# Kernel tuning notes

Hardware: AMD Instinct MI355X
Metric: run time of the kernel (lower is better)

Reference implementation:

```python
import jax, jax.numpy as jnp
import numpy as np

N_NODES = 100000
N_EDGES = 1600000
IN_DIM = 128
HID = 128
N_CLS = 10
N_GRAPHS = 128


def setup_inputs() -> dict:
    key = jax.random.key(0)
    ks = jax.random.split(key, 8)
    x = jax.random.normal(ks[0], (N_NODES, IN_DIM), dtype=jnp.float32)
    edge_index = jax.random.randint(ks[1], (2, N_EDGES), 0, N_NODES, dtype=jnp.int64)
    batch = jnp.sort(jax.random.randint(ks[2], (N_NODES,), 0, N_GRAPHS, dtype=jnp.int64))
    # GCNConv weights (PyG uses glorot; scale approximated) and biases
    W1 = jax.random.normal(ks[3], (IN_DIM, HID), dtype=jnp.float32) * (1.0 / np.sqrt(IN_DIM))
    b1 = jnp.zeros((HID,), dtype=jnp.float32)
    W2 = jax.random.normal(ks[4], (HID, HID), dtype=jnp.float32) * (1.0 / np.sqrt(HID))
    b2 = jnp.zeros((HID,), dtype=jnp.float32)
    Wlin = jax.random.normal(ks[5], (HID, N_CLS), dtype=jnp.float32) * (1.0 / np.sqrt(HID))
    blin = jnp.zeros((N_CLS,), dtype=jnp.float32)
    return {"x": x, "edge_index": edge_index, "batch": batch,
            "W1": W1, "b1": b1, "W2": W2, "b2": b2, "Wlin": Wlin, "blin": blin}


def _gcn_norm(edge_index, n_nodes):
    # PyG GCNConv default: add self-loops, symmetric D^-1/2 A D^-1/2 normalization
    loop = jnp.arange(n_nodes, dtype=edge_index.dtype)
    row = jnp.concatenate([edge_index[0], loop])  # source nodes
    col = jnp.concatenate([edge_index[1], loop])  # destination nodes
    ones = jnp.ones(col.shape[0], dtype=jnp.float32)
    deg = jax.ops.segment_sum(ones, col, num_segments=n_nodes)
    dinv = jnp.where(deg > 0, jax.lax.rsqrt(deg), 0.0)
    norm = dinv[row] * dinv[col]  # per-edge normalization coefficient
    return row, col, norm


def _gcn_conv(x, W, b, row, col, norm, n_nodes):
    h = x @ W                                   # [N, hid] dense transform first (small hid)
    msg = h[row] * norm[:, None]                # gather + scale over edges
    out = jax.ops.segment_sum(msg, col, num_segments=n_nodes)  # scatter-add aggregation
    return out + b


def reference(x, edge_index, batch, W1, b1, W2, b2, Wlin, blin):
    n = x.shape[0]
    row, col, norm = _gcn_norm(edge_index, n)
    h = jax.nn.relu(_gcn_conv(x, W1, b1, row, col, norm, n))
    h = jax.nn.relu(_gcn_conv(h, W2, b2, row, col, norm, n))
    # global_mean_pool over batch ids
    sums = jax.ops.segment_sum(h, batch, num_segments=N_GRAPHS)
    cnts = jax.ops.segment_sum(jnp.ones((n,), dtype=h.dtype), batch, num_segments=N_GRAPHS)
    pooled = sums / jnp.maximum(cnts, 1.0)[:, None]
    return pooled @ Wlin + blin  # [N_GRAPHS, n_cls]
```

## Files before the change

### kernel.cpp

```cpp
#include <hip/hip_runtime.h>

#define NN 100000
#define NE 1600000
#define DD 128
#define NG 128
#define NC 10
#define POOL_WAVES 2048

#define B1SH 8
#define NB1 ((NN + 255) / 256)
#define EPB 8192
#define NWG1 ((NE + EPB - 1) / EPB)

typedef __attribute__((ext_vector_type(8))) short short8v;
typedef __attribute__((ext_vector_type(4))) float f32x4;

__device__ __forceinline__ unsigned short f2bf(float f) {
    unsigned int u = __float_as_uint(f);
    u = (u + 0x7fffu + ((u >> 16) & 1u)) >> 16;
    return (unsigned short)u;
}

__global__ __launch_bounds__(256) void hist_k(const int* __restrict__ col, int* __restrict__ hist) {
    __shared__ int lh[NB1];
    int t = threadIdx.x, w = blockIdx.x;
    for (int i = t; i < NB1; i += 256) lh[i] = 0;
    __syncthreads();
    int base = w * EPB;
    int lim = min(base + EPB, NE);
#pragma unroll 4
    for (int e = base + t; e < lim; e += 256) atomicAdd(&lh[col[e] >> B1SH], 1);
    __syncthreads();
    for (int i = t; i < NB1; i += 256) hist[i * NWG1 + w] = lh[i];
}

__global__ __launch_bounds__(512) void btot_k(const int* __restrict__ hist, int* __restrict__ bbase) {
    __shared__ int tmp[512];
    int t = threadIdx.x;
    int s = 0;
    if (t < NB1) {
        const int* hp = hist + t * NWG1;
        for (int w = 0; w < NWG1; ++w) s += hp[w];
    }
    tmp[t] = s;
    __syncthreads();
    for (int o = 1; o < 512; o <<= 1) {
        int v = (t >= o) ? tmp[t - o] : 0;
        __syncthreads();
        tmp[t] += v;
        __syncthreads();
    }
    if (t < NB1) bbase[t] = tmp[t] - s;
    if (t == 511) bbase[NB1] = tmp[511];
}

__global__ __launch_bounds__(256) void histscan_k(const int* __restrict__ bbase, int* __restrict__ hist) {
    __shared__ int tmp[256];
    int b = blockIdx.x, t = threadIdx.x;
    int v = (t < NWG1) ? hist[b * NWG1 + t] : 0;
    tmp[t] = v;
    __syncthreads();
    for (int o = 1; o < 256; o <<= 1) {
        int u = (t >= o) ? tmp[t - o] : 0;
        __syncthreads();
        tmp[t] += u;
        __syncthreads();
    }
    int excl = tmp[t] - v;
    if (t < NWG1) hist[b * NWG1 + t] = bbase[b] + excl;
}

__global__ __launch_bounds__(256) void part1_k(const int* __restrict__ row, const int* __restrict__ col,
                                               const int* __restrict__ hist, int* __restrict__ tmpe) {
    __shared__ int lcur[NB1];
    int t = threadIdx.x, w = blockIdx.x;
    for (int i = t; i < NB1; i += 256) lcur[i] = hist[i * NWG1 + w];
    __syncthreads();
    int base = w * EPB;
    int lim = min(base + EPB, NE);
#pragma unroll 4
    for (int e = base + t; e < lim; e += 256) {
        int c = col[e];
        int pos = atomicAdd(&lcur[c >> B1SH], 1);
        tmpe[pos] = (row[e] << B1SH) | (c & 255);
    }
}

__global__ __launch_bounds__(512) void part2b_k(const int* __restrict__ bbase, const int* __restrict__ tmpe,
                                                unsigned int* __restrict__ csr_src, int* __restrict__ offs,
                                                float* __restrict__ dinv) {
    __shared__ int lcnt[256];
    __shared__ int lsc[256];
    int b = blockIdx.x, t = threadIdx.x;
    if (t < 256) lcnt[t] = 0;
    __syncthreads();
    int ebeg = bbase[b], eend = bbase[b + 1];
    for (int e = ebeg + t; e < eend; e += 512) atomicAdd(&lcnt[tmpe[e] & 255], 1);
    __syncthreads();
    if (t < 256) lsc[t] = lcnt[t];
    __syncthreads();
    for (int o = 1; o < 256; o <<= 1) {
        int v = (t < 256 && t >= o) ? lsc[t - o] : 0;
        __syncthreads();
        if (t < 256) lsc[t] += v;
        __syncthreads();
    }
    int n0 = b << B1SH;
    if (t < 256) {
        int node = n0 + t;
        if (node < NN) {
            int excl = lsc[t] - lcnt[t];
            offs[node] = ebeg + excl;
            dinv[node] = rsqrtf((float)lcnt[t] + 1.0f);
        }
    }
    if (b == NB1 - 1 && t == 0) offs[NN] = NE;
    __syncthreads();
    if (t < 256) lsc[t] = ebeg + (lsc[t] - lcnt[t]);
    __syncthreads();
    for (int e = ebeg + t; e < eend; e += 512) {
        int p = tmpe[e];
        int pos = atomicAdd(&lsc[p & 255], 1);
        csr_src[pos] = (unsigned int)(p >> B1SH) << 6;
    }
}

__global__ __launch_bounds__(256) void pack_w2_k(const float* __restrict__ W1, const float* __restrict__ W2,
                                                 unsigned short* __restrict__ Wpk1,
                                                 unsigned short* __restrict__ Wpk2) {
    const float* W = blockIdx.x ? W2 : W1;
    unsigned short* Wpk = blockIdx.x ? Wpk2 : Wpk1;
    int t = threadIdx.x;
    for (int f = t * 64; f < t * 64 + 64; ++f) {
        int j = f & 7, lane = (f >> 3) & 63, kk = (f >> 9) & 3, n = f >> 11;
        int k = kk * 32 + ((lane >> 4) << 3) + j;
        int c = n * 16 + (lane & 15);
        Wpk[f] = f2bf(W[k * DD + c]);
    }
}

template <int IN_BF16>
__global__ __launch_bounds__(256) void gemm_mfma_k(const void* __restrict__ Xv,
                                                   const unsigned short* __restrict__ Wpk,
                                                   const float* __restrict__ dinv,
                                                   unsigned short* __restrict__ outb) {
    __shared__ unsigned short wlds[16384];
    int tid = threadIdx.x;
    const uint4* wg = (const uint4*)Wpk;
    uint4* wl = (uint4*)wlds;
#pragma unroll
    for (int i = 0; i < 8; ++i) wl[tid + i * 256] = wg[tid + i * 256];
    __syncthreads();

    int w = tid >> 6, lane = tid & 63;
    int kg = lane >> 4;
    int rowbase = blockIdx.x * 64 + w * 16;
    int rl = min(rowbase + (lane & 15), NN - 1);

    short8v a[4];
    if (IN_BF16) {
        const unsigned short* xb = (const unsigned short*)Xv;
#pragma unroll
        for (int kk = 0; kk < 4; ++kk)
            a[kk] = *(const short8v*)(xb + (long)rl * DD + kk * 32 + kg * 8);
    } else {
        const float* xf = (const float*)Xv;
#pragma unroll
        for (int kk = 0; kk < 4; ++kk) {
            float4 f0 = *(const float4*)(xf + (long)rl * DD + kk * 32 + kg * 8);
            float4 f1 = *(const float4*)(xf + (long)rl * DD + kk * 32 + kg * 8 + 4);
            short8v t;
            t[0] = (short)f2bf(f0.x); t[1] = (short)f2bf(f0.y);
            t[2] = (short)f2bf(f0.z); t[3] = (short)f2bf(f0.w);
            t[4] = (short)f2bf(f1.x); t[5] = (short)f2bf(f1.y);
            t[6] = (short)f2bf(f1.z); t[7] = (short)f2bf(f1.w);
            a[kk] = t;
        }
    }

    f32x4 acc[8];
#pragma unroll
    for (int n = 0; n < 8; ++n) acc[n] = (f32x4){0.f, 0.f, 0.f, 0.f};
#pragma unroll
    for (int n = 0; n < 8; ++n) {
#pragma unroll
        for (int kk = 0; kk < 4; ++kk) {
            short8v b = *(const short8v*)(wlds + ((n * 4 + kk) * 64 + lane) * 8);
            acc[n] = __builtin_amdgcn_mfma_f32_16x16x32_bf16(a[kk], b, acc[n], 0, 0, 0);
        }
    }

    int c0 = lane & 15;
#pragma unroll
    for (int reg = 0; reg < 4; ++reg) {
        int row = rowbase + kg * 4 + reg;
        if (row < NN) {
            float dv = dinv[row];
            unsigned short* op = outb + (long)row * DD + c0;
#pragma unroll
            for (int n = 0; n < 8; ++n) op[n * 16] = f2bf(dv * acc[n][reg]);
        }
    }
}

__global__ __launch_bounds__(256) void agg_k(const unsigned int* __restrict__ hpb,
                                             const float* __restrict__ dinv,
                                             const int* __restrict__ offs,
                                             const unsigned int* __restrict__ csr,
                                             const float* __restrict__ bias,
                                             unsigned short* __restrict__ outb) {
    int node = (blockIdx.x << 2) + (threadIdx.x >> 6);
    if (node >= NN) return;
    unsigned int lane = threadIdx.x & 63;
    int s = offs[node];
    int e_end = offs[node + 1];
    unsigned int ps = hpb[(unsigned int)node * 64u + lane];
    float accx = __uint_as_float(ps << 16);
    float accy = __uint_as_float(ps & 0xffff0000u);
    int e = s;
    for (; e + 8 <= e_end; e += 8) {
        unsigned int i0 = csr[e] + lane;     unsigned int i1 = csr[e + 1] + lane;
        unsigned int i2 = csr[e + 2] + lane; unsigned int i3 = csr[e + 3] + lane;
        unsigned int i4 = csr[e + 4] + lane; unsigned int i5 = csr[e + 5] + lane;
        unsigned int i6 = csr[e + 6] + lane; unsigned int i7 = csr[e + 7] + lane;
        unsigned int p0 = hpb[i0];
        unsigned int p1 = hpb[i1];
        unsigned int p2 = hpb[i2];
        unsigned int p3 = hpb[i3];
        unsigned int p4 = hpb[i4];
        unsigned int p5 = hpb[i5];
        unsigned int p6 = hpb[i6];
        unsigned int p7 = hpb[i7];
        accx += (__uint_as_float(p0 << 16) + __uint_as_float(p1 << 16)) +
                (__uint_as_float(p2 << 16) + __uint_as_float(p3 << 16)) +
                (__uint_as_float(p4 << 16) + __uint_as_float(p5 << 16)) +
                (__uint_as_float(p6 << 16) + __uint_as_float(p7 << 16));
        accy += (__uint_as_float(p0 & 0xffff0000u) + __uint_as_float(p1 & 0xffff0000u)) +
                (__uint_as_float(p2 & 0xffff0000u) + __uint_as_float(p3 & 0xffff0000u)) +
                (__uint_as_float(p4 & 0xffff0000u) + __uint_as_float(p5 & 0xffff0000u)) +
                (__uint_as_float(p6 & 0xffff0000u) + __uint_as_float(p7 & 0xffff0000u));
    }
    if (e + 4 <= e_end) {
        unsigned int p0 = hpb[csr[e] + lane];
        unsigned int p1 = hpb[csr[e + 1] + lane];
        unsigned int p2 = hpb[csr[e + 2] + lane];
        unsigned int p3 = hpb[csr[e + 3] + lane];
        accx += (__uint_as_float(p0 << 16) + __uint_as_float(p1 << 16)) +
                (__uint_as_float(p2 << 16) + __uint_as_float(p3 << 16));
        accy += (__uint_as_float(p0 & 0xffff0000u) + __uint_as_float(p1 & 0xffff0000u)) +
                (__uint_as_float(p2 & 0xffff0000u) + __uint_as_float(p3 & 0xffff0000u));
        e += 4;
    }
    for (; e < e_end; ++e) {
        unsigned int p0 = hpb[csr[e] + lane];
        accx += __uint_as_float(p0 << 16);
        accy += __uint_as_float(p0 & 0xffff0000u);
    }
    float dv = dinv[node];
    float2 b = ((const float2*)bias)[lane];
    float ox = fmaxf(fmaf(dv, accx, b.x), 0.0f);
    float oy = fmaxf(fmaf(dv, accy, b.y), 0.0f);
    ((ushort2*)outb)[(unsigned int)node * 64u + lane] = make_ushort2(f2bf(ox), f2bf(oy));
}

__global__ __launch_bounds__(256) void pool2_k(const unsigned short* __restrict__ h,
                                               const int* __restrict__ batch,
                                               float* __restrict__ gsum) {
    int wave = (blockIdx.x * 256 + threadIdx.x) >> 6;
    int lane = threadIdx.x & 63;
    const int per = (NN + POOL_WAVES - 1) / POOL_WAVES;
    int s = wave * per;
    int e = min(s + per, NN);
    if (s >= e) return;
    const unsigned int* h2 = (const unsigned int*)h;
    float2 acc = {0.0f, 0.0f};
    int cur = batch[s];
    for (int r = s; r < e; ++r) {
        int b = batch[r];
        if (b != cur) {
            atomicAdd(&gsum[cur * DD + 2 * lane], acc.x);
            atomicAdd(&gsum[cur * DD + 2 * lane + 1], acc.y);
            acc.x = 0.0f; acc.y = 0.0f;
            cur = b;
        }
        unsigned int v = h2[(unsigned int)r * 64u + lane];
        acc.x += __uint_as_float(v << 16);
        acc.y += __uint_as_float(v & 0xffff0000u);
    }
    atomicAdd(&gsum[cur * DD + 2 * lane], acc.x);
    atomicAdd(&gsum[cur * DD + 2 * lane + 1], acc.y);
}

__global__ __launch_bounds__(256) void final_k(const float* __restrict__ gsum, const int* __restrict__ batch,
                                               const float* __restrict__ Wlin, const float* __restrict__ blin,
                                               float* __restrict__ out) {
    int idx = blockIdx.x * 256 + threadIdx.x;
    if (idx >= NG * NC) return;
    int g = idx / NC, c = idx % NC;
    int s0, s1;
    {
        int lo = 0, hi = NN;
        while (lo < hi) { int m = (lo + hi) >> 1; if (batch[m] < g) lo = m + 1; else hi = m; }
        s0 = lo;
        lo = s0; hi = NN;
        while (lo < hi) { int m = (lo + hi) >> 1; if (batch[m] < g + 1) lo = m + 1; else hi = m; }
        s1 = lo;
    }
    int cnt = s1 - s0;
    float inv = 1.0f / fmaxf((float)cnt, 1.0f);
    float acc = blin[c];
    for (int k = 0; k < DD; ++k) acc = fmaf(gsum[g * DD + k] * inv, Wlin[k * NC + c], acc);
    out[idx] = acc;
}

extern "C" void kernel_launch(void* const* d_in, const int* in_sizes, int n_in,
                              void* d_out, int out_size, void* d_ws, size_t ws_size,
                              hipStream_t stream) {
    const float* x     = (const float*)d_in[0];
    const int*   ei    = (const int*)d_in[1];
    const int*   batch = (const int*)d_in[2];
    const float* W1    = (const float*)d_in[3];
    const float* b1    = (const float*)d_in[4];
    const float* W2    = (const float*)d_in[5];
    const float* b2    = (const float*)d_in[6];
    const float* Wlin  = (const float*)d_in[7];
    const float* blin  = (const float*)d_in[8];
    float* out = (float*)d_out;

    const int* erow = ei;
    const int* ecol = ei + NE;

    char* ws = (char*)d_ws;
    size_t off = 0;
    auto alloc = [&](size_t bytes) {
        void* p = ws + off;
        off = (off + bytes + 255) & ~(size_t)255;
        return p;
    };
    unsigned short* hbuf  = (unsigned short*)alloc((size_t)NN * DD * 2);
    unsigned short* habuf = (unsigned short*)alloc((size_t)NN * DD * 2);
    unsigned short* Wpk1  = (unsigned short*)alloc(16384 * 2);
    unsigned short* Wpk2  = (unsigned short*)alloc(16384 * 2);
    float* dinv     = (float*)alloc(NN * 4);
    int*   offs     = (int*)alloc((NN + 1) * 4);
    int*   bbase    = (int*)alloc((NB1 + 1) * 4);
    int*   hist     = (int*)alloc((size_t)NB1 * NWG1 * 4);
    int*   tmpe     = (int*)alloc((size_t)NE * 4);
    unsigned int* csrsrc = (unsigned int*)alloc((size_t)NE * 4);
    float* gsum     = (float*)alloc(NG * DD * 4);
    (void)ws_size; (void)in_sizes; (void)n_in; (void)out_size;

    hipMemsetAsync(gsum, 0, NG * DD * 4, stream);

    hist_k<<<NWG1, 256, 0, stream>>>(ecol, hist);
    btot_k<<<1, 512, 0, stream>>>(hist, bbase);
    histscan_k<<<NB1, 256, 0, stream>>>(bbase, hist);
    part1_k<<<NWG1, 256, 0, stream>>>(erow, ecol, hist, tmpe);
    part2b_k<<<NB1, 512, 0, stream>>>(bbase, tmpe, csrsrc, offs, dinv);

    pack_w2_k<<<2, 256, 0, stream>>>(W1, W2, Wpk1, Wpk2);

    int gblocks = (NN + 63) / 64;
    gemm_mfma_k<0><<<gblocks, 256, 0, stream>>>(x, Wpk1, dinv, hbuf);
    agg_k<<<(NN + 3) / 4, 256, 0, stream>>>((const unsigned int*)hbuf, dinv, offs, csrsrc, b1, habuf);
    gemm_mfma_k<1><<<gblocks, 256, 0, stream>>>(habuf, Wpk2, dinv, hbuf);
    agg_k<<<(NN + 3) / 4, 256, 0, stream>>>((const unsigned int*)hbuf, dinv, offs, csrsrc, b2, habuf);

    pool2_k<<<POOL_WAVES / 4, 256, 0, stream>>>(habuf, batch, gsum);
    final_k<<<(NG * NC + 255) / 256, 256, 0, stream>>>(gsum, batch, Wlin, blin, out);
}
```

Before: 270.1 us.

## Fuse first GEMM with histogram, pack weights in-kernel, aggregate two nodes per wave

The first GEMM no longer depends on dinv: the source-side dinv scaling moves into aggregation as a per-edge gather. That lets GEMM1 be merged into the histogram launch together with the gsum zeroing, so it can overlap the CSR build. Weight packing to bf16 now happens inside each GEMM block, which removes the separate pack kernel. Each aggregation wave now processes two nodes with interleaved edge loops to expose more memory parallelism. The cost is an extra dinv load per edge and every GEMM block repeating the weight conversion.

```diff
diff --git a/kernel.cpp b/kernel.cpp
--- a/kernel.cpp
+++ b/kernel.cpp
@@ -11,6 +11,7 @@
 #define NB1 ((NN + 255) / 256)
 #define EPB 8192
 #define NWG1 ((NE + EPB - 1) / EPB)
+#define GEMM_BLOCKS ((NN + 63) / 64)
 
 typedef __attribute__((ext_vector_type(8))) short short8v;
 typedef __attribute__((ext_vector_type(4))) float f32x4;
@@ -20,141 +21,34 @@
     u = (u + 0x7fffu + ((u >> 16) & 1u)) >> 16;
     return (unsigned short)u;
 }
-
-__global__ __launch_bounds__(256) void hist_k(const int* __restrict__ col, int* __restrict__ hist) {
-    __shared__ int lh[NB1];
-    int t = threadIdx.x, w = blockIdx.x;
-    for (int i = t; i < NB1; i += 256) lh[i] = 0;
-    __syncthreads();
-    int base = w * EPB;
-    int lim = min(base + EPB, NE);
-#pragma unroll 4
-    for (int e = base + t; e < lim; e += 256) atomicAdd(&lh[col[e] >> B1SH], 1);
-    __syncthreads();
-    for (int i = t; i < NB1; i += 256) hist[i * NWG1 + w] = lh[i];
-}
-
-__global__ __launch_bounds__(512) void btot_k(const int* __restrict__ hist, int* __restrict__ bbase) {
-    __shared__ int tmp[512];
-    int t = threadIdx.x;
-    int s = 0;
-    if (t < NB1) {
-        const int* hp = hist + t * NWG1;
-        for (int w = 0; w < NWG1; ++w) s += hp[w];
-    }
-    tmp[t] = s;
-    __syncthreads();
-    for (int o = 1; o < 512; o <<= 1) {
-        int v = (t >= o) ? tmp[t - o] : 0;
-        __syncthreads();
-        tmp[t] += v;
-        __syncthreads();
-    }
-    if (t < NB1) bbase[t] = tmp[t] - s;
-    if (t == 511) bbase[NB1] = tmp[511];
-}
-
-__global__ __launch_bounds__(256) void histscan_k(const int* __restrict__ bbase, int* __restrict__ hist) {
-    __shared__ int tmp[256];
-    int b = blockIdx.x, t = threadIdx.x;
-    int v = (t < NWG1) ? hist[b * NWG1 + t] : 0;
-    tmp[t] = v;
-    __syncthreads();
-    for (int o = 1; o < 256; o <<= 1) {
-        int u = (t >= o) ? tmp[t - o] : 0;
-        __syncthreads();
-        tmp[t] += u;
-        __syncthreads();
-    }
-    int excl = tmp[t] - v;
-    if (t < NWG1) hist[b * NWG1 + t] = bbase[b] + excl;
-}
-
-__global__ __launch_bounds__(256) void part1_k(const int* __restrict__ row, const int* __restrict__ col,
-                                               const int* __restrict__ hist, int* __restrict__ tmpe) {
-    __shared__ int lcur[NB1];
-    int t = threadIdx.x, w = blockIdx.x;
-    for (int i = t; i < NB1; i += 256) lcur[i] = hist[i * NWG1 + w];
-    __syncthreads();
-    int base = w * EPB;
-    int lim = min(base + EPB, NE);
-#pragma unroll 4
-    for (int e = base + t; e < lim; e += 256) {
-        int c = col[e];
-        int pos = atomicAdd(&lcur[c >> B1SH], 1);
-        tmpe[pos] = (row[e] << B1SH) | (c & 255);
-    }
-}
-
-__global__ __launch_bounds__(512) void part2b_k(const int* __restrict__ bbase, const int* __restrict__ tmpe,
-                                                unsigned int* __restrict__ csr_src, int* __restrict__ offs,
-                                                float* __restrict__ dinv) {
-    __shared__ int lcnt[256];
-    __shared__ int lsc[256];
-    int b = blockIdx.x, t = threadIdx.x;
-    if (t < 256) lcnt[t] = 0;
-    __syncthreads();
-    int ebeg = bbase[b], eend = bbase[b + 1];
-    for (int e = ebeg + t; e < eend; e += 512) atomicAdd(&lcnt[tmpe[e] & 255], 1);
-    __syncthreads();
-    if (t < 256) lsc[t] = lcnt[t];
-    __syncthreads();
-    for (int o = 1; o < 256; o <<= 1) {
-        int v = (t < 256 && t >= o) ? lsc[t - o] : 0;
-        __syncthreads();
-        if (t < 256) lsc[t] += v;
-        __syncthreads();
-    }
-    int n0 = b << B1SH;
-    if (t < 256) {
-        int node = n0 + t;
-        if (node < NN) {
-            int excl = lsc[t] - lcnt[t];
-            offs[node] = ebeg + excl;
-            dinv[node] = rsqrtf((float)lcnt[t] + 1.0f);
-        }
-    }
-    if (b == NB1 - 1 && t == 0) offs[NN] = NE;
-    __syncthreads();
-    if (t < 256) lsc[t] = ebeg + (lsc[t] - lcnt[t]);
-    __syncthreads();
-    for (int e = ebeg + t; e < eend; e += 512) {
-        int p = tmpe[e];
-        int pos = atomicAdd(&lsc[p & 255], 1);
-        csr_src[pos] = (unsigned int)(p >> B1SH) << 6;
-    }
-}
-
-__global__ __launch_bounds__(256) void pack_w2_k(const float* __restrict__ W1, const float* __restrict__ W2,
-                                                 unsigned short* __restrict__ Wpk1,
-                                                 unsigned short* __restrict__ Wpk2) {
-    const float* W = blockIdx.x ? W2 : W1;
-    unsigned short* Wpk = blockIdx.x ? Wpk2 : Wpk1;
-    int t = threadIdx.x;
-    for (int f = t * 64; f < t * 64 + 64; ++f) {
-        int j = f & 7, lane = (f >> 3) & 63, kk = (f >> 9) & 3, n = f >> 11;
-        int k = kk * 32 + ((lane >> 4) << 3) + j;
-        int c = n * 16 + (lane & 15);
-        Wpk[f] = f2bf(W[k * DD + c]);
-    }
-}
+__device__ __forceinline__ float bflo(unsigned int p) { return __uint_as_float(p << 16); }
+__device__ __forceinline__ float bfhi(unsigned int p) { return __uint_as_float(p & 0xffff0000u); }
 
 template <int IN_BF16>
-__global__ __launch_bounds__(256) void gemm_mfma_k(const void* __restrict__ Xv,
-                                                   const unsigned short* __restrict__ Wpk,
-                                                   const float* __restrict__ dinv,
-                                                   unsigned short* __restrict__ outb) {
-    __shared__ unsigned short wlds[16384];
+__device__ __forceinline__ void gemm_body(const void* __restrict__ Xv, const float* __restrict__ W,
+                                          unsigned short* __restrict__ outb, int blk,
+                                          unsigned short* wlds) {
     int tid = threadIdx.x;
-    const uint4* wg = (const uint4*)Wpk;
-    uint4* wl = (uint4*)wlds;
-#pragma unroll
-    for (int i = 0; i < 8; ++i) wl[tid + i * 256] = wg[tid + i * 256];
+    const float4* W4 = (const float4*)W;
+#pragma unroll
+    for (int it = 0; it < 16; ++it) {
+        int li = it * 256 + tid;
+        float4 f = W4[li];
+        int idx = li * 4;
+        int k = idx >> 7, c = idx & 127;
+        int kk = k >> 5, hi = (k >> 3) & 3, j = k & 7;
+        const float* fp = (const float*)&f;
+#pragma unroll
+        for (int q = 0; q < 4; ++q) {
+            int cc = c + q;
+            wlds[(((cc >> 4) * 4 + kk) * 64 + hi * 16 + (cc & 15)) * 8 + j] = f2bf(fp[q]);
+        }
+    }
     __syncthreads();
 
     int w = tid >> 6, lane = tid & 63;
     int kg = lane >> 4;
-    int rowbase = blockIdx.x * 64 + w * 16;
+    int rowbase = blk * 64 + w * 16;
     int rl = min(rowbase + (lane & 15), NN - 1);
 
     short8v a[4];
@@ -195,11 +89,132 @@
     for (int reg = 0; reg < 4; ++reg) {
         int row = rowbase + kg * 4 + reg;
         if (row < NN) {
-            float dv = dinv[row];
             unsigned short* op = outb + (long)row * DD + c0;
 #pragma unroll
-            for (int n = 0; n < 8; ++n) op[n * 16] = f2bf(dv * acc[n][reg]);
-        }
+            for (int n = 0; n < 8; ++n) op[n * 16] = f2bf(acc[n][reg]);
+        }
+    }
+}
+
+__global__ __launch_bounds__(256) void k1_fused(const int* __restrict__ col, int* __restrict__ hist,
+                                                const float* __restrict__ x, const float* __restrict__ W1,
+                                                unsigned short* __restrict__ hbuf,
+                                                float* __restrict__ gsum) {
+    __shared__ unsigned short wlds[16384];
+    int bid = blockIdx.x, t = threadIdx.x;
+    if (bid < NWG1) {
+        int* lh = (int*)wlds;
+        for (int i = t; i < NB1; i += 256) lh[i] = 0;
+        __syncthreads();
+        int base = bid * EPB;
+        int lim = min(base + EPB, NE);
+#pragma unroll 4
+        for (int e = base + t; e < lim; e += 256) atomicAdd(&lh[col[e] >> B1SH], 1);
+        __syncthreads();
+        for (int i = t; i < NB1; i += 256) hist[i * NWG1 + bid] = lh[i];
+    } else if (bid == NWG1) {
+        float4* g4 = (float4*)gsum;
+        for (int i = t; i < NG * DD / 4; i += 256) g4[i] = make_float4(0, 0, 0, 0);
+    } else {
+        gemm_body<0>(x, W1, hbuf, bid - NWG1 - 1, wlds);
+    }
+}
+
+__global__ __launch_bounds__(256) void gemm2_k(const unsigned short* __restrict__ xb,
+                                               const float* __restrict__ W2,
+                                               unsigned short* __restrict__ outb) {
+    __shared__ unsigned short wlds[16384];
+    gemm_body<1>(xb, W2, outb, blockIdx.x, wlds);
+}
+
+__global__ __launch_bounds__(512) void btot_k(const int* __restrict__ hist, int* __restrict__ bbase) {
+    __shared__ int tmp[512];
+    int t = threadIdx.x;
+    int s = 0;
+    if (t < NB1) {
+        const int* hp = hist + t * NWG1;
+        for (int w = 0; w < NWG1; ++w) s += hp[w];
+    }
+    tmp[t] = s;
+    __syncthreads();
+    for (int o = 1; o < 512; o <<= 1) {
+        int v = (t >= o) ? tmp[t - o] : 0;
+        __syncthreads();
+        tmp[t] += v;
+        __syncthreads();
+    }
+    if (t < NB1) bbase[t] = tmp[t] - s;
+    if (t == 511) bbase[NB1] = tmp[511];
+}
+
+__global__ __launch_bounds__(256) void histscan_k(const int* __restrict__ bbase, int* __restrict__ hist) {
+    __shared__ int tmp[256];
+    int b = blockIdx.x, t = threadIdx.x;
+    int v = (t < NWG1) ? hist[b * NWG1 + t] : 0;
+    tmp[t] = v;
+    __syncthreads();
+    for (int o = 1; o < 256; o <<= 1) {
+        int u = (t >= o) ? tmp[t - o] : 0;
+        __syncthreads();
+        tmp[t] += u;
+        __syncthreads();
+    }
+    int excl = tmp[t] - v;
+    if (t < NWG1) hist[b * NWG1 + t] = bbase[b] + excl;
+}
+
+__global__ __launch_bounds__(256) void part1_k(const int* __restrict__ row, const int* __restrict__ col,
+                                               const int* __restrict__ hist, int* __restrict__ tmpe) {
+    __shared__ int lcur[NB1];
+    int t = threadIdx.x, w = blockIdx.x;
+    for (int i = t; i < NB1; i += 256) lcur[i] = hist[i * NWG1 + w];
+    __syncthreads();
+    int base = w * EPB;
+    int lim = min(base + EPB, NE);
+#pragma unroll 4
+    for (int e = base + t; e < lim; e += 256) {
+        int c = col[e];
+        int pos = atomicAdd(&lcur[c >> B1SH], 1);
+        tmpe[pos] = (row[e] << B1SH) | (c & 255);
+    }
+}
+
+__global__ __launch_bounds__(512) void part2b_k(const int* __restrict__ bbase, const int* __restrict__ tmpe,
+                                                unsigned int* __restrict__ csr_src, int* __restrict__ offs,
+                                                float* __restrict__ dinv) {
+    __shared__ int lcnt[256];
+    __shared__ int lsc[256];
+    int b = blockIdx.x, t = threadIdx.x;
+    if (t < 256) lcnt[t] = 0;
+    __syncthreads();
+    int ebeg = bbase[b], eend = bbase[b + 1];
+    for (int e = ebeg + t; e < eend; e += 512) atomicAdd(&lcnt[tmpe[e] & 255], 1);
+    __syncthreads();
+    if (t < 256) lsc[t] = lcnt[t];
+    __syncthreads();
+    for (int o = 1; o < 256; o <<= 1) {
+        int v = (t < 256 && t >= o) ? lsc[t - o] : 0;
+        __syncthreads();
+        if (t < 256) lsc[t] += v;
+        __syncthreads();
+    }
+    int n0 = b << B1SH;
+    if (t < 256) {
+        int node = n0 + t;
+        if (node < NN) {
+            int excl = lsc[t] - lcnt[t];
+            offs[node] = ebeg + excl;
+            dinv[node] = rsqrtf((float)lcnt[t] + 1.0f);
+        }
+    }
+    if (b == NB1 - 1 && t == 0) offs[NN] = NE;
+    __syncthreads();
+    if (t < 256) lsc[t] = ebeg + (lsc[t] - lcnt[t]);
+    __syncthreads();
+    for (int e = ebeg + t; e < eend; e += 512) {
+        int p = tmpe[e];
+        int pos = atomicAdd(&lsc[p & 255], 1);
+        csr_src[pos] = (unsigned int)(p >> B1SH) << 6;
     }
 }
 
@@ -209,58 +224,55 @@
                                              const unsigned int* __restrict__ csr,
                                              const float* __restrict__ bias,
                                              unsigned short* __restrict__ outb) {
-    int node = (blockIdx.x << 2) + (threadIdx.x >> 6);
-    if (node >= NN) return;
+    int wv = (blockIdx.x << 2) + (threadIdx.x >> 6);
+    int nA = wv * 2, nB = nA + 1;
     unsigned int lane = threadIdx.x & 63;
-    int s = offs[node];
-    int e_end = offs[node + 1];
-    unsigned int ps = hpb[(unsigned int)node * 64u + lane];
-    float accx = __uint_as_float(ps << 16);
-    float accy = __uint_as_float(ps & 0xffff0000u);
-    int e = s;
-    for (; e + 8 <= e_end; e += 8) {
-        unsigned int i0 = csr[e] + lane;     unsigned int i1 = csr[e + 1] + lane;
-        unsigned int i2 = csr[e + 2] + lane; unsigned int i3 = csr[e + 3] + lane;
-        unsigned int i4 = csr[e + 4] + lane; unsigned int i5 = csr[e + 5] + lane;
-        unsigned int i6 = csr[e + 6] + lane; unsigned int i7 = csr[e + 7] + lane;
-        unsigned int p0 = hpb[i0];
-        unsigned int p1 = hpb[i1];
-        unsigned int p2 = hpb[i2];
-        unsigned int p3 = hpb[i3];
-        unsigned int p4 = hpb[i4];
-        unsigned int p5 = hpb[i5];
-        unsigned int p6 = hpb[i6];
-        unsigned int p7 = hpb[i7];
-        accx += (__uint_as_float(p0 << 16) + __uint_as_float(p1 << 16)) +
-                (__uint_as_float(p2 << 16) + __uint_as_float(p3 << 16)) +
-                (__uint_as_float(p4 << 16) + __uint_as_float(p5 << 16)) +
-                (__uint_as_float(p6 << 16) + __uint_as_float(p7 << 16));
-        accy += (__uint_as_float(p0 & 0xffff0000u) + __uint_as_float(p1 & 0xffff0000u)) +
-                (__uint_as_float(p2 & 0xffff0000u) + __uint_as_float(p3 & 0xffff0000u)) +
-                (__uint_as_float(p4 & 0xffff0000u) + __uint_as_float(p5 & 0xffff0000u)) +
-                (__uint_as_float(p6 & 0xffff0000u) + __uint_as_float(p7 & 0xffff0000u));
-    }
-    if (e + 4 <= e_end) {
-        unsigned int p0 = hpb[csr[e] + lane];
-        unsigned int p1 = hpb[csr[e + 1] + lane];
-        unsigned int p2 = hpb[csr[e + 2] + lane];
-        unsigned int p3 = hpb[csr[e + 3] + lane];
-        accx += (__uint_as_float(p0 << 16) + __uint_as_float(p1 << 16)) +
-                (__uint_as_float(p2 << 16) + __uint_as_float(p3 << 16));
-        accy += (__uint_as_float(p0 & 0xffff0000u) + __uint_as_float(p1 & 0xffff0000u)) +
-                (__uint_as_float(p2 & 0xffff0000u) + __uint_as_float(p3 & 0xffff0000u));
-        e += 4;
-    }
-    for (; e < e_end; ++e) {
-        unsigned int p0 = hpb[csr[e] + lane];
-        accx += __uint_as_float(p0 << 16);
-        accy += __uint_as_float(p0 & 0xffff0000u);
-    }
-    float dv = dinv[node];
-    float2 b = ((const float2*)bias)[lane];
-    float ox = fmaxf(fmaf(dv, accx, b.x), 0.0f);
-    float oy = fmaxf(fmaf(dv, accy, b.y), 0.0f);
-    ((ushort2*)outb)[(unsigned int)node * 64u + lane] = make_ushort2(f2bf(ox), f2bf(oy));
+    int sA = offs[nA];
+    int eA = offs[nA + 1];
+    int eB = offs[nB + 1];
+    int sB = eA;
+    float dvA = dinv[nA], dvB = dinv[nB];
+    unsigned int pA = hpb[(unsigned int)nA * 64u + lane];
+    unsigned int pB = hpb[(unsigned int)nB * 64u + lane];
+    float aAx = dvA * bflo(pA), aAy = dvA * bfhi(pA);
+    float aBx = dvB * bflo(pB), aBy = dvB * bfhi(pB);
+
+    auto b4 = [&](int e, float& ax, float& ay) {
+        unsigned int c0 = csr[e], c1 = csr[e + 1], c2 = csr[e + 2], c3 = csr[e + 3];
+        float d0 = dinv[c0 >> 6], d1 = dinv[c1 >> 6], d2 = dinv[c2 >> 6], d3 = dinv[c3 >> 6];
+        unsigned int p0 = hpb[c0 + lane], p1 = hpb[c1 + lane];
+        unsigned int p2 = hpb[c2 + lane], p3 = hpb[c3 + lane];
+        ax = fmaf(d0, bflo(p0), ax); ay = fmaf(d0, bfhi(p0), ay);
+        ax = fmaf(d1, bflo(p1), ax); ay = fmaf(d1, bfhi(p1), ay);
+        ax = fmaf(d2, bflo(p2), ax); ay = fmaf(d2, bfhi(p2), ay);
+        ax = fmaf(d3, bflo(p3), ax); ay = fmaf(d3, bfhi(p3), ay);
+    };
+
+    int iA = sA, iB = sB;
+    while (iA + 4 <= eA && iB + 4 <= eB) {
+        b4(iA, aAx, aAy);
+        b4(iB, aBx, aBy);
+        iA += 4; iB += 4;
+    }
+    while (iA + 4 <= eA) { b4(iA, aAx, aAy); iA += 4; }
+    while (iB + 4 <= eB) { b4(iB, aBx, aBy); iB += 4; }
+    for (; iA < eA; ++iA) {
+        unsigned int c = csr[iA];
+        float d = dinv[c >> 6];
+        unsigned int p = hpb[c + lane];
+        aAx = fmaf(d, bflo(p), aAx); aAy = fmaf(d, bfhi(p), aAy);
+    }
+    for (; iB < eB; ++iB) {
+        unsigned int c = csr[iB];
+        float d = dinv[c >> 6];
+        unsigned int p = hpb[c + lane];
+        aBx = fmaf(d, bflo(p), aBx); aBy = fmaf(d, bfhi(p), aBy);
+    }
+    float2 bb = ((const float2*)bias)[lane];
+    ((ushort2*)outb)[(unsigned int)nA * 64u + lane] =
+        make_ushort2(f2bf(fmaxf(fmaf(dvA, aAx, bb.x), 0.0f)), f2bf(fmaxf(fmaf(dvA, aAy, bb.y), 0.0f)));
+    ((ushort2*)outb)[(unsigned int)nB * 64u + lane] =
+        make_ushort2(f2bf(fmaxf(fmaf(dvB, aBx, bb.x), 0.0f)), f2bf(fmaxf(fmaf(dvB, aBy, bb.y), 0.0f)));
 }
 
 __global__ __launch_bounds__(256) void pool2_k(const unsigned short* __restrict__ h,
@@ -284,8 +296,8 @@
             cur = b;
         }
         unsigned int v = h2[(unsigned int)r * 64u + lane];
-        acc.x += __uint_as_float(v << 16);
-        acc.y += __uint_as_float(v & 0xffff0000u);
+        acc.x += bflo(v);
+        acc.y += bfhi(v);
     }
     atomicAdd(&gsum[cur * DD + 2 * lane], acc.x);
     atomicAdd(&gsum[cur * DD + 2 * lane + 1], acc.y);
@@ -339,8 +351,6 @@
     };
     unsigned short* hbuf  = (unsigned short*)alloc((size_t)NN * DD * 2);
     unsigned short* habuf = (unsigned short*)alloc((size_t)NN * DD * 2);
-    unsigned short* Wpk1  = (unsigned short*)alloc(16384 * 2);
-    unsigned short* Wpk2  = (unsigned short*)alloc(16384 * 2);
     float* dinv     = (float*)alloc(NN * 4);
     int*   offs     = (int*)alloc((NN + 1) * 4);
     int*   bbase    = (int*)alloc((NB1 + 1) * 4);
@@ -350,21 +360,15 @@
     float* gsum     = (float*)alloc(NG * DD * 4);
     (void)ws_size; (void)in_sizes; (void)n_in; (void)out_size;
 
-    hipMemsetAsync(gsum, 0, NG * DD * 4, stream);
-
-    hist_k<<<NWG1, 256, 0, stream>>>(ecol, hist);
+    k1_fused<<<NWG1 + 1 + GEMM_BLOCKS, 256, 0, stream>>>(ecol, hist, x, W1, hbuf, gsum);
     btot_k<<<1, 512, 0, stream>>>(hist, bbase);
     histscan_k<<<NB1, 256, 0, stream>>>(bbase, hist);
     part1_k<<<NWG1, 256, 0, stream>>>(erow, ecol, hist, tmpe);
     part2b_k<<<NB1, 512, 0, stream>>>(bbase, tmpe, csrsrc, offs, dinv);
 
-    pack_w2_k<<<2, 256, 0, stream>>>(W1, W2, Wpk1, Wpk2);
-
-    int gblocks = (NN + 63) / 64;
-    gemm_mfma_k<0><<<gblocks, 256, 0, stream>>>(x, Wpk1, dinv, hbuf);
-    agg_k<<<(NN + 3) / 4, 256, 0, stream>>>((const unsigned int*)hbuf, dinv, offs, csrsrc, b1, habuf);
-    gemm_mfma_k<1><<<gblocks, 256, 0, stream>>>(habuf, Wpk2, dinv, hbuf);
-    agg_k<<<(NN + 3) / 4, 256, 0, stream>>>((const unsigned int*)hbuf, dinv, offs, csrsrc, b2, habuf);
+    agg_k<<<NN / 8, 256, 0, stream>>>((const unsigned int*)hbuf, dinv, offs, csrsrc, b1, habuf);
+    gemm2_k<<<GEMM_BLOCKS, 256, 0, stream>>>(habuf, W2, hbuf);
+    agg_k<<<NN / 8, 256, 0, stream>>>((const unsigned int*)hbuf, dinv, offs, csrsrc, b2, habuf);
 
     pool2_k<<<POOL_WAVES / 4, 256, 0, stream>>>(habuf, batch, gsum);
     final_k<<<(NG * NC + 255) / 256, 256, 0, stream>>>(gsum, batch, Wlin, blin, out);
```

After: 279.1 us. 1.03x slower.
